# Performance work log

Measured on AMD Instinct MI355X. Metric: run time of the kernel, lower is better.

The kernel has to match this reference:

```python
import jax, jax.numpy as jnp
import numpy as np

D_MODEL, H, D_K, D_V, M = 1024, 8, 128, 128, 16
B, NQ, NK = 8, 1024, 1024


def setup_inputs() -> dict:
    key = jax.random.key(0)
    ks = jax.random.split(key, 12)
    f = jnp.float32
    inp = {
        "queries": jax.random.normal(ks[0], (B, NQ, D_MODEL), f),
        "keys": jax.random.normal(ks[1], (B, NK, D_MODEL), f),
        "values": jax.random.normal(ks[2], (B, NK, D_MODEL), f),
        "attention_mask": jax.random.bernoulli(ks[3], 0.15, (B, H, NQ, NK)),
        # linear weights stored (in, out) so y = x @ W + b
        "Wq": jax.random.normal(ks[4], (D_MODEL, H * D_K), f) * (2.0 / D_MODEL) ** 0.5,
        "bq": jnp.zeros((H * D_K,), f),
        "Wk": jax.random.normal(ks[5], (D_MODEL, H * D_K), f) * (2.0 / D_MODEL) ** 0.5,
        "bk": jnp.zeros((H * D_K,), f),
        "Wv": jax.random.normal(ks[6], (D_MODEL, H * D_V), f) * (2.0 / D_MODEL) ** 0.5,
        "bv": jnp.zeros((H * D_V,), f),
        "Wo": jax.random.normal(ks[7], (H * D_V, D_MODEL), f) * (2.0 / D_MODEL) ** 0.5,
        "bo": jnp.zeros((D_MODEL,), f),
        "m_k": jax.random.normal(ks[8], (1, M, H * D_K), f) * (1.0 / D_K),
        "m_v": jax.random.normal(ks[9], (1, M, H * D_V), f) * (1.0 / M),
    }
    return inp


def reference(queries, keys, values, attention_mask, Wq, bq, Wk, bk, Wv, bv, Wo, bo, m_k, m_v):
    b, nq, _ = queries.shape
    nk = keys.shape[1]
    scale = 1.0 / np.sqrt(D_K).astype(np.float32)

    q = (queries @ Wq + bq).reshape(b, nq, H, D_K)                # (b,nq,h,dk)
    mk = np.sqrt(D_K).astype(np.float32) * jnp.broadcast_to(m_k, (b, M, H * D_K))
    mv = np.sqrt(M).astype(np.float32) * jnp.broadcast_to(m_v, (b, M, H * D_V))
    k = jnp.concatenate([keys @ Wk + bk, mk], axis=1).reshape(b, nk + M, H, D_K)
    v = jnp.concatenate([values @ Wv + bv, mv], axis=1).reshape(b, nk + M, H, D_V)

    att = jnp.einsum("bqhd,bkhd->bhqk", q, k) * scale             # (b,h,nq,nk+m)
    # mask only the real-key slice; memory slots are never masked
    full_mask = jnp.concatenate(
        [attention_mask, jnp.zeros((b, H, nq, M), dtype=bool)], axis=-1)
    att = jnp.where(full_mask, -jnp.inf, att)
    att = jax.nn.softmax(att, axis=-1)

    out = jnp.einsum("bhqk,bkhd->bqhd", att, v).reshape(b, nq, H * D_V)
    out = out @ Wo + bo
    return out, att.reshape(-1, nq, nk)
```

## Files before the change

### kernel.cpp

```cpp
#include <hip/hip_runtime.h>


typedef unsigned short u16;
typedef unsigned int   u32;
typedef _Float16 f16x8 __attribute__((ext_vector_type(8)));
typedef short    s16x8 __attribute__((ext_vector_type(8)));
typedef float    f32x4 __attribute__((ext_vector_type(4)));

#define MFMA_F16(a, b, c) __builtin_amdgcn_mfma_f32_16x16x32_f16((a), (b), (c), 0, 0, 0)

#define NQS    1024
#define NKM    1040
#define KSP    1056
#define SCALE_QK 0.088388347648318447f

__device__ __forceinline__ u16 f2h(float f) {
  _Float16 h = (_Float16)f;
  return __builtin_bit_cast(u16, h);
}
__device__ __forceinline__ f16x8 ld_h8(const u16* p) {
  s16x8 r = *(const s16x8*)p;
  return __builtin_bit_cast(f16x8, r);
}

__global__ void cvt16_kernel(const float* __restrict__ in, u16* __restrict__ out, int n4) {
  for (int i = blockIdx.x * blockDim.x + threadIdx.x; i < n4;
       i += gridDim.x * blockDim.x) {
    float4 v = ((const float4*)in)[i];
    ushort4 h;
    h.x = f2h(v.x); h.y = f2h(v.y); h.z = f2h(v.z); h.w = f2h(v.w);
    ((ushort4*)out)[i] = h;
  }
}

__global__ __launch_bounds__(256)
void wtrans16_kernel(const float* __restrict__ w, u16* __restrict__ t16) {
  __shared__ float t[64][65];
  const int bx = blockIdx.x & 15;
  const int by = blockIdx.x >> 4;
  const int r = threadIdx.x >> 4, c4 = threadIdx.x & 15;
#pragma unroll
  for (int i = 0; i < 4; ++i) {
    const int row = bx * 64 + r + i * 16;
    float4 v = *(const float4*)&w[row * 1024 + by * 64 + c4 * 4];
    t[r + i * 16][c4 * 4 + 0] = v.x;
    t[r + i * 16][c4 * 4 + 1] = v.y;
    t[r + i * 16][c4 * 4 + 2] = v.z;
    t[r + i * 16][c4 * 4 + 3] = v.w;
  }
  __syncthreads();
  const int l = threadIdx.x & 63, og = threadIdx.x >> 6;
#pragma unroll
  for (int j = 0; j < 16; ++j) {
    const int o_local = og + j * 4;
    t16[(by * 64 + o_local) * 1024 + bx * 64 + l] = f2h(t[l][o_local]);
  }
}

__global__ void mk_fill_kernel(const float* __restrict__ m_k, u16* __restrict__ kh) {
  int idx = blockIdx.x * 256 + threadIdx.x;
  int b = idx >> 15, h = (idx >> 12) & 7, ko = (idx >> 7) & 31, dk = idx & 127;
  float v = 0.f;
  if (ko < 16) v = 11.313708498984760f * m_k[ko * 1024 + h * 128 + dk];
  kh[((b * 8 + h) * KSP + 1024 + ko) * 128 + dk] = f2h(v);
}

__global__ void mv_fill_kernel(const float* __restrict__ m_v, u16* __restrict__ vt) {
  int idx = blockIdx.x * 256 + threadIdx.x;
  int b = idx >> 15, h = (idx >> 12) & 7, dv = (idx >> 5) & 127, ko = idx & 31;
  float v = (ko < 16) ? 4.0f * m_v[ko * 1024 + h * 128 + dv] : 0.f;
  vt[((b * 8 + h) * 128 + dv) * KSP + 1024 + ko] = f2h(v);
}

__global__ void maskbits_kernel(const int* __restrict__ mask, u32* __restrict__ mbits) {
  const int lane = threadIdx.x & 63;
  const int nwave = (gridDim.x * blockDim.x) >> 6;
  int wid = (blockIdx.x * blockDim.x + threadIdx.x) >> 6;
  for (int g = wid; g < 262144; g += nwave) {
    const int4 m = *(const int4*)&mask[(size_t)g * 256 + lane * 4];
    u32 nib = (m.x ? 1u : 0u) | (m.y ? 2u : 0u) | (m.z ? 4u : 0u) | (m.w ? 8u : 0u);
    u32 v = nib << ((lane & 7) * 4);
    v |= __shfl_xor(v, 1);
    v |= __shfl_xor(v, 2);
    v |= __shfl_xor(v, 4);
    if ((lane & 7) == 0) {
      const int row = g >> 2;
      const int word = ((g & 3) << 3) + (lane >> 3);
      mbits[row * 33 + word] = v;
    }
  }
}

__global__ void maskfill_kernel(u32* __restrict__ mbits) {
  int idx = blockIdx.x * 256 + threadIdx.x;
  mbits[idx * 33 + 32] = 0xFFFF0000u;
}

__device__ __forceinline__ void stage_tile(const u16* __restrict__ gbase,
                                           u16* sbase, int w, int lane) {
#pragma unroll
  for (int i = 0; i < 4; ++i) {
    const u16* src = gbase + (w * 32 + i * 8 + (lane >> 3)) * 1024 + (lane & 7) * 8;
    u16* dst = sbase + (w * 32 + i * 8) * 64;
    __builtin_amdgcn_global_load_lds(
        (const __attribute__((address_space(1))) void*)src,
        (__attribute__((address_space(3))) void*)dst, 16, 0, 0);
  }
}

enum { EPI_Q16 = 0, EPI_K16 = 1, EPI_VT = 2, EPI_OUT = 3 };

template <int EPI>
__global__ __launch_bounds__(256)
void gemm_kernel(const u16* __restrict__ A, const u16* __restrict__ B,
                 const float* __restrict__ bias,
                 u16* __restrict__ oH, float* __restrict__ oF) {
  __shared__ u16 sA[128 * 64];
  __shared__ u16 sB[128 * 64];
  const int lane = threadIdx.x & 63, w = threadIdx.x >> 6;
  const int bm = blockIdx.x & 63, bn = blockIdx.x >> 6;
  const int wr = w >> 1, wc = w & 1;

  f32x4 acc[4][4];
  const f32x4 fz = {0.f, 0.f, 0.f, 0.f};
#pragma unroll
  for (int m = 0; m < 4; ++m)
#pragma unroll
    for (int n = 0; n < 4; ++n) acc[m][n] = fz;

  for (int kt = 0; kt < 16; ++kt) {
    const int kb = kt * 64;
    stage_tile(A + bm * 128 * 1024 + kb, sA, w, lane);
    stage_tile(B + bn * 128 * 1024 + kb, sB, w, lane);
    __syncthreads();
    const int ro = lane & 15;
#pragma unroll
    for (int kk = 0; kk < 2; ++kk) {
      const int co = kk * 32 + (lane >> 4) * 8;
      f16x8 a[4], b[4];
#pragma unroll
      for (int m = 0; m < 4; ++m) a[m] = ld_h8(&sA[(wr * 64 + m * 16 + ro) * 64 + co]);
#pragma unroll
      for (int n = 0; n < 4; ++n) b[n] = ld_h8(&sB[(wc * 64 + n * 16 + ro) * 64 + co]);
#pragma unroll
      for (int m = 0; m < 4; ++m)
#pragma unroll
        for (int n = 0; n < 4; ++n)
          acc[m][n] = MFMA_F16(a[m], b[n], acc[m][n]);
    }
    __syncthreads();
  }

#pragma unroll
  for (int m = 0; m < 4; ++m)
#pragma unroll
    for (int n = 0; n < 4; ++n) {
      const int row0 = bm * 128 + wr * 64 + m * 16 + ((lane >> 4) << 2);
      const int col = bn * 128 + wc * 64 + n * 16 + (lane & 15);
      const float bv = bias[col];
#pragma unroll
      for (int r = 0; r < 4; ++r) {
        const float y = acc[m][n][r] + bv;
        const int row = row0 + r;
        if constexpr (EPI == EPI_Q16) {
          oH[row * 1024 + col] = f2h(y);
        } else if constexpr (EPI == EPI_K16) {
          const int b = row >> 10, key = row & 1023;
          oH[((b * 8 + (col >> 7)) * KSP + key) * 128 + (col & 127)] = f2h(y);
        } else if constexpr (EPI == EPI_VT) {
          const int b = row >> 10, key = row & 1023;
          oH[((b * 8 + (col >> 7)) * 128 + (col & 127)) * KSP + key] = f2h(y);
        } else {
          oF[row * 1024 + col] = y;
        }
      }
    }
}

__global__ __launch_bounds__(256, 4)
void attn_kernel(const u16* __restrict__ qh, const u16* __restrict__ kh,
                 const u16* __restrict__ vt, const u32* __restrict__ mbits,
                 float* __restrict__ att, u16* __restrict__ obuf) {
  __shared__ __align__(16) u16 sK[64 * 128];
  __shared__ __align__(16) u16 sVt[128 * 40];
  __shared__ __align__(16) float sAtt[4][16][36];
  const int tid = threadIdx.x;
  const int lane = tid & 63, w = tid >> 6;

  const int d = blockIdx.x;
  const int j = d >> 3;
  const int bh = (d & 7) * 8 + (j >> 4);
  const int qblk = j & 15;
  const int h = bh & 7;
  const int b = bh >> 3;
  const int qrow0 = qblk * 64 + w * 16;
  const int grow0 = b * NQS + qrow0;
  const int ro = lane & 15, go = lane >> 4;

  f16x8 qf[4];
#pragma unroll
  for (int kk = 0; kk < 4; ++kk)
    qf[kk] = ld_h8(&qh[(grow0 + ro) * 1024 + h * 128 + kk * 32 + go * 8]);

  const u16* khb = kh + (size_t)bh * KSP * 128;
  const u16* vtb = vt + (size_t)bh * 128 * KSP;
  const u32* mbb = mbits + (size_t)bh * NQS * 33;
  float* attb = att + (size_t)(bh * NQS + qrow0) * NKM;

  const int r_k  = tid >> 4;
  const int cb_k = (tid & 15) * 16;
  const u16* kp0 = khb + r_k * 128 + (cb_k >> 1);
  const int dk0 = r_k * 256 + (cb_k ^ ((r_k & 7) << 4));

  const f32x4 fz = {0.f, 0.f, 0.f, 0.f};
  float lsum[4] = {0.f, 0.f, 0.f, 0.f};

  {
    s16x8 ra = *(const s16x8*)(kp0);
    s16x8 rb = *(const s16x8*)(kp0 + 16 * 128);
    s16x8 rc = *(const s16x8*)(kp0 + 32 * 128);
    s16x8 rd = *(const s16x8*)(kp0 + 48 * 128);
    for (int c = 0; c < 16; ++c) {
      __syncthreads();
      *(s16x8*)((char*)sK + dk0)         = ra;
      *(s16x8*)((char*)sK + dk0 + 4096)  = rb;
      *(s16x8*)((char*)sK + dk0 + 8192)  = rc;
      *(s16x8*)((char*)sK + dk0 + 12288) = rd;
      if (c < 15) {
        const u16* p = kp0 + (c + 1) * 64 * 128;
        ra = *(const s16x8*)(p);
        rb = *(const s16x8*)(p + 16 * 128);
        rc = *(const s16x8*)(p + 32 * 128);
        rd = *(const s16x8*)(p + 48 * 128);
      } else {
        ra = *(const s16x8*)(kp0 + 1024 * 128);
        rb = *(const s16x8*)(kp0 + 1040 * 128);
      }
      __syncthreads();
      u32 mw0[4], mw1[4];
#pragma unroll
      for (int r = 0; r < 4; ++r) {
        const int row = qrow0 + (go << 2) + r;
        mw0[r] = mbb[row * 33 + 2 * c];
        mw1[r] = mbb[row * 33 + 2 * c + 1];
      }
#pragma unroll
      for (int t = 0; t < 4; ++t) {
        f32x4 s = fz;
        const int rr = t * 16 + ro;
        const int sw = (rr & 7) << 4;
        __builtin_amdgcn_s_setprio(1);
#pragma unroll
        for (int kk = 0; kk < 4; ++kk) {
          const int off = rr * 256 + ((kk * 64 + go * 16) ^ sw);
          s = MFMA_F16(qf[kk], ld_h8((const u16*)((const char*)sK + off)), s);
        }
        __builtin_amdgcn_s_setprio(0);
        const int bit = (t & 1) * 16 + ro;
#pragma unroll
        for (int r = 0; r < 4; ++r) {
          const u32 mw = (t < 2) ? mw0[r] : mw1[r];
          const bool dead = (mw >> bit) & 1;
          const float e = dead ? 0.f : __expf(s[r] * SCALE_QK);
          lsum[r] += e;
        }
      }
    }
    __syncthreads();
    *(s16x8*)((char*)sK + dk0)        = ra;
    *(s16x8*)((char*)sK + dk0 + 4096) = rb;
    __syncthreads();
    u32 mwt[4];
#pragma unroll
    for (int r = 0; r < 4; ++r)
      mwt[r] = mbb[(qrow0 + (go << 2) + r) * 33 + 32];
#pragma unroll
    for (int t = 0; t < 2; ++t) {
      f32x4 s = fz;
      const int rr = t * 16 + ro;
      const int sw = (rr & 7) << 4;
#pragma unroll
      for (int kk = 0; kk < 4; ++kk) {
        const int off = rr * 256 + ((kk * 64 + go * 16) ^ sw);
        s = MFMA_F16(qf[kk], ld_h8((const u16*)((const char*)sK + off)), s);
      }
      const int bit = t * 16 + ro;
#pragma unroll
      for (int r = 0; r < 4; ++r) {
        const bool dead = (mwt[r] >> bit) & 1;
        lsum[r] += dead ? 0.f : __expf(s[r] * SCALE_QK);
      }
    }
  }

  float inv[4];
#pragma unroll
  for (int r = 0; r < 4; ++r) {
    lsum[r] += __shfl_xor(lsum[r], 1);
    lsum[r] += __shfl_xor(lsum[r], 2);
    lsum[r] += __shfl_xor(lsum[r], 4);
    lsum[r] += __shfl_xor(lsum[r], 8);
    inv[r] = 1.0f / lsum[r];
  }

  f32x4 oacc[8];
#pragma unroll
  for (int n = 0; n < 8; ++n) oacc[n] = fz;

  int vr[3], vcs[3];
  bool vok[3];
#pragma unroll
  for (int p = 0; p < 3; ++p) {
    const int t = p * 256 + tid;
    vok[p] = (t < 640);
    const int rr = vok[p] ? (t / 5) : 0;
    const int m5 = t - rr * 5;
    vr[p] = rr;
    vcs[p] = (m5 == 4 || !vok[p]) ? 0 : m5 * 8;
  }

  s16x8 rkh0, rkh1, rv0, rv1, rv2;
  rkh0 = *(const s16x8*)(kp0);
  rkh1 = *(const s16x8*)(kp0 + 16 * 128);
  rv0 = *(const s16x8*)(vtb + (size_t)vr[0] * KSP + vcs[0]);
  rv1 = *(const s16x8*)(vtb + (size_t)vr[1] * KSP + vcs[1]);
  if (vok[2]) rv2 = *(const s16x8*)(vtb + (size_t)vr[2] * KSP + vcs[2]);

  for (int c = 0; c < 33; ++c) {
    const int kb = c * 32;
    __syncthreads();
    *(s16x8*)((char*)sK + dk0)        = rkh0;
    *(s16x8*)((char*)sK + dk0 + 4096) = rkh1;
    *(s16x8*)((char*)sVt + tid * 16)         = rv0;
    *(s16x8*)((char*)sVt + (256 + tid) * 16) = rv1;
    if (vok[2]) *(s16x8*)((char*)sVt + (512 + tid) * 16) = rv2;
    if (c < 32) {
      const int nkb = (c + 1) * 32;
      rkh0 = *(const s16x8*)(kp0 + nkb * 128);
      rkh1 = *(const s16x8*)(kp0 + (nkb + 16) * 128);
      rv0 = *(const s16x8*)(vtb + (size_t)vr[0] * KSP + nkb + vcs[0]);
      rv1 = *(const s16x8*)(vtb + (size_t)vr[1] * KSP + nkb + vcs[1]);
      if (vok[2]) rv2 = *(const s16x8*)(vtb + (size_t)vr[2] * KSP + nkb + vcs[2]);
    }
    __syncthreads();

    u32 mw[4];
#pragma unroll
    for (int r = 0; r < 4; ++r) mw[r] = mbb[(qrow0 + (go << 2) + r) * 33 + c];

#pragma unroll
    for (int t = 0; t < 2; ++t) {
      f32x4 s = fz;
      const int rr = t * 16 + ro;
      const int sw = (rr & 7) << 4;
      __builtin_amdgcn_s_setprio(1);
#pragma unroll
      for (int kk = 0; kk < 4; ++kk) {
        const int off = rr * 256 + ((kk * 64 + go * 16) ^ sw);
        s = MFMA_F16(qf[kk], ld_h8((const u16*)((const char*)sK + off)), s);
      }
      __builtin_amdgcn_s_setprio(0);
      const int key_in = t * 16 + ro;
#pragma unroll
      for (int r = 0; r < 4; ++r) {
        const int lrow = (go << 2) + r;
        const bool dead = (mw[r] >> key_in) & 1;
        const float e = dead ? 0.f : __expf(s[r] * SCALE_QK);
        sAtt[w][lrow][t * 16 + ro] = e * inv[r];
      }
    }

    {
      const int arow = lane >> 2, cg = lane & 3;
      if (kb + cg * 8 < NKM) {
        f32x4 v0 = *(const f32x4*)&sAtt[w][arow][cg * 8];
        f32x4 v1 = *(const f32x4*)&sAtt[w][arow][cg * 8 + 4];
        float* dst = attb + (size_t)arow * NKM + kb + cg * 8;
        *(f32x4*)dst = v0;
        *(f32x4*)(dst + 4) = v1;
      }
    }

    {
      f32x4 p0 = *(const f32x4*)&sAtt[w][ro][go * 8];
      f32x4 p1 = *(const f32x4*)&sAtt[w][ro][go * 8 + 4];
      f16x8 pa;
      pa[0] = (_Float16)p0[0]; pa[1] = (_Float16)p0[1];
      pa[2] = (_Float16)p0[2]; pa[3] = (_Float16)p0[3];
      pa[4] = (_Float16)p1[0]; pa[5] = (_Float16)p1[1];
      pa[6] = (_Float16)p1[2]; pa[7] = (_Float16)p1[3];
      __builtin_amdgcn_s_setprio(1);
#pragma unroll
      for (int n = 0; n < 8; ++n) {
        f16x8 vb = ld_h8((const u16*)((const char*)sVt + (n * 16 + ro) * 80 + go * 16));
        oacc[n] = MFMA_F16(pa, vb, oacc[n]);
      }
      __builtin_amdgcn_s_setprio(0);
    }
  }

#pragma unroll
  for (int n = 0; n < 8; ++n)
#pragma unroll
    for (int r = 0; r < 4; ++r)
      obuf[(grow0 + (go << 2) + r) * 1024 + h * 128 + n * 16 + ro] = f2h(oacc[n][r]);
}

extern "C" void kernel_launch(void* const* d_in, const int* in_sizes, int n_in,
                              void* d_out, int out_size, void* d_ws, size_t ws_size,
                              hipStream_t stream) {
  const float* queries = (const float*)d_in[0];
  const float* keys    = (const float*)d_in[1];
  const float* values  = (const float*)d_in[2];
  const int*   mask    = (const int*)d_in[3];
  const float* Wq = (const float*)d_in[4];
  const float* bq = (const float*)d_in[5];
  const float* Wk = (const float*)d_in[6];
  const float* bk = (const float*)d_in[7];
  const float* Wv = (const float*)d_in[8];
  const float* bv = (const float*)d_in[9];
  const float* Wo = (const float*)d_in[10];
  const float* bo = (const float*)d_in[11];
  const float* m_k = (const float*)d_in[12];
  const float* m_v = (const float*)d_in[13];

  if (ws_size < 135528448) return;

  char* ws = (char*)d_ws;
  u16* xq  = (u16*)(ws + 0);
  u16* xk  = (u16*)(ws + 16777216);
  u16* xv  = (u16*)(ws + 33554432);
  u16* wq  = (u16*)(ws + 50331648);
  u16* wk  = (u16*)(ws + 52428800);
  u16* wv  = (u16*)(ws + 54525952);
  u16* wo  = (u16*)(ws + 56623104);
  u16* q16 = (u16*)(ws + 58720256);
  u16* k16 = (u16*)(ws + 75497472);
  u16* vt  = (u16*)(ws + 92798976);
  u16* obuf= (u16*)(ws + 110100480);
  u32* mbits=(u32*)(ws + 126877696);

  float* out = (float*)d_out;
  float* att = out + 8388608;

  cvt16_kernel<<<2048, 256, 0, stream>>>(queries, xq, 2097152);
  cvt16_kernel<<<2048, 256, 0, stream>>>(keys,    xk, 2097152);
  cvt16_kernel<<<2048, 256, 0, stream>>>(values,  xv, 2097152);
  wtrans16_kernel<<<256, 256, 0, stream>>>(Wq, wq);
  wtrans16_kernel<<<256, 256, 0, stream>>>(Wk, wk);
  wtrans16_kernel<<<256, 256, 0, stream>>>(Wv, wv);
  wtrans16_kernel<<<256, 256, 0, stream>>>(Wo, wo);
  gemm_kernel<EPI_Q16><<<512, 256, 0, stream>>>(xq, wq, bq, q16, nullptr);
  gemm_kernel<EPI_K16><<<512, 256, 0, stream>>>(xk, wk, bk, k16, nullptr);
  gemm_kernel<EPI_VT> <<<512, 256, 0, stream>>>(xv, wv, bv, vt,  nullptr);
  maskbits_kernel<<<2048, 256, 0, stream>>>(mask, mbits);
  maskfill_kernel<<<256, 256, 0, stream>>>(mbits);
  mk_fill_kernel<<<1024, 256, 0, stream>>>(m_k, k16);
  mv_fill_kernel<<<1024, 256, 0, stream>>>(m_v, vt);
  attn_kernel<<<1024, 256, 0, stream>>>(q16, k16, vt, mbits, att, obuf);
  gemm_kernel<EPI_OUT><<<512, 256, 0, stream>>>(obuf, wo, bo, nullptr, out);
}
```

Baseline: 409.5 us.

## Use 64-key chunks in attention PV pass and pad keys to uniform tiles

Pads the key dimension to 1088 and the mask row stride to 34 words, so both attention passes run 17 uniform 64-key chunks with no special tail block. The second pass now stages 64 keys of K and V per barrier pair instead of 32, halving the number of block synchronisations. The output tile is staged through LDS so the obuf stores become 16-byte writes. The extra registers and LDS lower the occupancy hint from 4 to 3 blocks per CU, and the padding adds some wasted MFMA work on masked-out keys.

```diff
diff --git a/kernel.cpp b/kernel.cpp
--- a/kernel.cpp
+++ b/kernel.cpp
@@ -11,7 +11,8 @@
 
 #define NQS    1024
 #define NKM    1040
-#define KSP    1056
+#define KSP    1088
+#define MW     34
 #define SCALE_QK 0.088388347648318447f
 
 __device__ __forceinline__ u16 f2h(float f) {
@@ -59,17 +60,19 @@
 
 __global__ void mk_fill_kernel(const float* __restrict__ m_k, u16* __restrict__ kh) {
   int idx = blockIdx.x * 256 + threadIdx.x;
-  int b = idx >> 15, h = (idx >> 12) & 7, ko = (idx >> 7) & 31, dk = idx & 127;
+  int bh = idx >> 13, ko = (idx >> 7) & 63, dk = idx & 127;
+  int h = bh & 7;
   float v = 0.f;
   if (ko < 16) v = 11.313708498984760f * m_k[ko * 1024 + h * 128 + dk];
-  kh[((b * 8 + h) * KSP + 1024 + ko) * 128 + dk] = f2h(v);
+  kh[((size_t)bh * KSP + 1024 + ko) * 128 + dk] = f2h(v);
 }
 
 __global__ void mv_fill_kernel(const float* __restrict__ m_v, u16* __restrict__ vt) {
   int idx = blockIdx.x * 256 + threadIdx.x;
-  int b = idx >> 15, h = (idx >> 12) & 7, dv = (idx >> 5) & 127, ko = idx & 31;
+  int bh = idx >> 13, dv = (idx >> 6) & 127, ko = idx & 63;
+  int h = bh & 7;
   float v = (ko < 16) ? 4.0f * m_v[ko * 1024 + h * 128 + dv] : 0.f;
-  vt[((b * 8 + h) * 128 + dv) * KSP + 1024 + ko] = f2h(v);
+  vt[((size_t)bh * 128 + dv) * KSP + 1024 + ko] = f2h(v);
 }
 
 __global__ void maskbits_kernel(const int* __restrict__ mask, u32* __restrict__ mbits) {
@@ -86,14 +89,15 @@
     if ((lane & 7) == 0) {
       const int row = g >> 2;
       const int word = ((g & 3) << 3) + (lane >> 3);
-      mbits[row * 33 + word] = v;
+      mbits[row * MW + word] = v;
     }
   }
 }
 
 __global__ void maskfill_kernel(u32* __restrict__ mbits) {
   int idx = blockIdx.x * 256 + threadIdx.x;
-  mbits[idx * 33 + 32] = 0xFFFF0000u;
+  mbits[idx * MW + 32] = 0xFFFF0000u;
+  mbits[idx * MW + 33] = 0xFFFFFFFFu;
 }
 
 __device__ __forceinline__ void stage_tile(const u16* __restrict__ gbase,
@@ -166,10 +170,10 @@
           oH[row * 1024 + col] = f2h(y);
         } else if constexpr (EPI == EPI_K16) {
           const int b = row >> 10, key = row & 1023;
-          oH[((b * 8 + (col >> 7)) * KSP + key) * 128 + (col & 127)] = f2h(y);
+          oH[((size_t)(b * 8 + (col >> 7)) * KSP + key) * 128 + (col & 127)] = f2h(y);
         } else if constexpr (EPI == EPI_VT) {
           const int b = row >> 10, key = row & 1023;
-          oH[((b * 8 + (col >> 7)) * 128 + (col & 127)) * KSP + key] = f2h(y);
+          oH[((size_t)(b * 8 + (col >> 7)) * 128 + (col & 127)) * KSP + key] = f2h(y);
         } else {
           oF[row * 1024 + col] = y;
         }
@@ -177,12 +181,12 @@
     }
 }
 
-__global__ __launch_bounds__(256, 4)
+__global__ __launch_bounds__(256, 3)
 void attn_kernel(const u16* __restrict__ qh, const u16* __restrict__ kh,
                  const u16* __restrict__ vt, const u32* __restrict__ mbits,
                  float* __restrict__ att, u16* __restrict__ obuf) {
   __shared__ __align__(16) u16 sK[64 * 128];
-  __shared__ __align__(16) u16 sVt[128 * 40];
+  __shared__ __align__(16) u16 sV[128 * 72];
   __shared__ __align__(16) float sAtt[4][16][36];
   const int tid = threadIdx.x;
   const int lane = tid & 63, w = tid >> 6;
@@ -204,45 +208,46 @@
 
   const u16* khb = kh + (size_t)bh * KSP * 128;
   const u16* vtb = vt + (size_t)bh * 128 * KSP;
-  const u32* mbb = mbits + (size_t)bh * NQS * 33;
+  const u32* mbb = mbits + (size_t)bh * NQS * MW;
   float* attb = att + (size_t)(bh * NQS + qrow0) * NKM;
 
   const int r_k  = tid >> 4;
   const int cb_k = (tid & 15) * 16;
   const u16* kp0 = khb + r_k * 128 + (cb_k >> 1);
   const int dk0 = r_k * 256 + (cb_k ^ ((r_k & 7) << 4));
+  const int vrow[4] = {(0 * 256 + tid) >> 3, (1 * 256 + tid) >> 3,
+                       (2 * 256 + tid) >> 3, (3 * 256 + tid) >> 3};
+  const int vc8[4]  = {(0 * 256 + tid) & 7, (1 * 256 + tid) & 7,
+                       (2 * 256 + tid) & 7, (3 * 256 + tid) & 7};
 
   const f32x4 fz = {0.f, 0.f, 0.f, 0.f};
   float lsum[4] = {0.f, 0.f, 0.f, 0.f};
 
   {
-    s16x8 ra = *(const s16x8*)(kp0);
-    s16x8 rb = *(const s16x8*)(kp0 + 16 * 128);
-    s16x8 rc = *(const s16x8*)(kp0 + 32 * 128);
-    s16x8 rd = *(const s16x8*)(kp0 + 48 * 128);
-    for (int c = 0; c < 16; ++c) {
+    s16x8 rk0 = *(const s16x8*)(kp0);
+    s16x8 rk1 = *(const s16x8*)(kp0 + 16 * 128);
+    s16x8 rk2 = *(const s16x8*)(kp0 + 32 * 128);
+    s16x8 rk3 = *(const s16x8*)(kp0 + 48 * 128);
+    for (int c = 0; c < 17; ++c) {
       __syncthreads();
-      *(s16x8*)((char*)sK + dk0)         = ra;
-      *(s16x8*)((char*)sK + dk0 + 4096)  = rb;
-      *(s16x8*)((char*)sK + dk0 + 8192)  = rc;
-      *(s16x8*)((char*)sK + dk0 + 12288) = rd;
-      if (c < 15) {
+      *(s16x8*)((char*)sK + dk0)         = rk0;
+      *(s16x8*)((char*)sK + dk0 + 4096)  = rk1;
+      *(s16x8*)((char*)sK + dk0 + 8192)  = rk2;
+      *(s16x8*)((char*)sK + dk0 + 12288) = rk3;
+      if (c < 16) {
         const u16* p = kp0 + (c + 1) * 64 * 128;
-        ra = *(const s16x8*)(p);
-        rb = *(const s16x8*)(p + 16 * 128);
-        rc = *(const s16x8*)(p + 32 * 128);
-        rd = *(const s16x8*)(p + 48 * 128);
-      } else {
-        ra = *(const s16x8*)(kp0 + 1024 * 128);
-        rb = *(const s16x8*)(kp0 + 1040 * 128);
+        rk0 = *(const s16x8*)(p);
+        rk1 = *(const s16x8*)(p + 16 * 128);
+        rk2 = *(const s16x8*)(p + 32 * 128);
+        rk3 = *(const s16x8*)(p + 48 * 128);
       }
       __syncthreads();
       u32 mw0[4], mw1[4];
 #pragma unroll
       for (int r = 0; r < 4; ++r) {
         const int row = qrow0 + (go << 2) + r;
-        mw0[r] = mbb[row * 33 + 2 * c];
-        mw1[r] = mbb[row * 33 + 2 * c + 1];
+        mw0[r] = mbb[row * MW + 2 * c];
+        mw1[r] = mbb[row * MW + 2 * c + 1];
       }
 #pragma unroll
       for (int t = 0; t < 4; ++t) {
@@ -261,34 +266,8 @@
         for (int r = 0; r < 4; ++r) {
           const u32 mw = (t < 2) ? mw0[r] : mw1[r];
           const bool dead = (mw >> bit) & 1;
-          const float e = dead ? 0.f : __expf(s[r] * SCALE_QK);
-          lsum[r] += e;
-        }
-      }
-    }
-    __syncthreads();
-    *(s16x8*)((char*)sK + dk0)        = ra;
-    *(s16x8*)((char*)sK + dk0 + 4096) = rb;
-    __syncthreads();
-    u32 mwt[4];
-#pragma unroll
-    for (int r = 0; r < 4; ++r)
-      mwt[r] = mbb[(qrow0 + (go << 2) + r) * 33 + 32];
-#pragma unroll
-    for (int t = 0; t < 2; ++t) {
-      f32x4 s = fz;
-      const int rr = t * 16 + ro;
-      const int sw = (rr & 7) << 4;
-#pragma unroll
-      for (int kk = 0; kk < 4; ++kk) {
-        const int off = rr * 256 + ((kk * 64 + go * 16) ^ sw);
-        s = MFMA_F16(qf[kk], ld_h8((const u16*)((const char*)sK + off)), s);
-      }
-      const int bit = t * 16 + ro;
-#pragma unroll
-      for (int r = 0; r < 4; ++r) {
-        const bool dead = (mwt[r] >> bit) & 1;
-        lsum[r] += dead ? 0.f : __expf(s[r] * SCALE_QK);
+          lsum[r] += dead ? 0.f : __expf(s[r] * SCALE_QK);
+        }
       }
     }
   }
@@ -307,103 +286,118 @@
 #pragma unroll
   for (int n = 0; n < 8; ++n) oacc[n] = fz;
 
-  int vr[3], vcs[3];
-  bool vok[3];
-#pragma unroll
-  for (int p = 0; p < 3; ++p) {
-    const int t = p * 256 + tid;
-    vok[p] = (t < 640);
-    const int rr = vok[p] ? (t / 5) : 0;
-    const int m5 = t - rr * 5;
-    vr[p] = rr;
-    vcs[p] = (m5 == 4 || !vok[p]) ? 0 : m5 * 8;
-  }
-
-  s16x8 rkh0, rkh1, rv0, rv1, rv2;
-  rkh0 = *(const s16x8*)(kp0);
-  rkh1 = *(const s16x8*)(kp0 + 16 * 128);
-  rv0 = *(const s16x8*)(vtb + (size_t)vr[0] * KSP + vcs[0]);
-  rv1 = *(const s16x8*)(vtb + (size_t)vr[1] * KSP + vcs[1]);
-  if (vok[2]) rv2 = *(const s16x8*)(vtb + (size_t)vr[2] * KSP + vcs[2]);
-
-  for (int c = 0; c < 33; ++c) {
-    const int kb = c * 32;
+  s16x8 rk0 = *(const s16x8*)(kp0);
+  s16x8 rk1 = *(const s16x8*)(kp0 + 16 * 128);
+  s16x8 rk2 = *(const s16x8*)(kp0 + 32 * 128);
+  s16x8 rk3 = *(const s16x8*)(kp0 + 48 * 128);
+  s16x8 rv0 = *(const s16x8*)(vtb + (size_t)vrow[0] * KSP + vc8[0] * 8);
+  s16x8 rv1 = *(const s16x8*)(vtb + (size_t)vrow[1] * KSP + vc8[1] * 8);
+  s16x8 rv2 = *(const s16x8*)(vtb + (size_t)vrow[2] * KSP + vc8[2] * 8);
+  s16x8 rv3 = *(const s16x8*)(vtb + (size_t)vrow[3] * KSP + vc8[3] * 8);
+
+  for (int c = 0; c < 17; ++c) {
     __syncthreads();
-    *(s16x8*)((char*)sK + dk0)        = rkh0;
-    *(s16x8*)((char*)sK + dk0 + 4096) = rkh1;
-    *(s16x8*)((char*)sVt + tid * 16)         = rv0;
-    *(s16x8*)((char*)sVt + (256 + tid) * 16) = rv1;
-    if (vok[2]) *(s16x8*)((char*)sVt + (512 + tid) * 16) = rv2;
-    if (c < 32) {
-      const int nkb = (c + 1) * 32;
-      rkh0 = *(const s16x8*)(kp0 + nkb * 128);
-      rkh1 = *(const s16x8*)(kp0 + (nkb + 16) * 128);
-      rv0 = *(const s16x8*)(vtb + (size_t)vr[0] * KSP + nkb + vcs[0]);
-      rv1 = *(const s16x8*)(vtb + (size_t)vr[1] * KSP + nkb + vcs[1]);
-      if (vok[2]) rv2 = *(const s16x8*)(vtb + (size_t)vr[2] * KSP + nkb + vcs[2]);
+    *(s16x8*)((char*)sK + dk0)         = rk0;
+    *(s16x8*)((char*)sK + dk0 + 4096)  = rk1;
+    *(s16x8*)((char*)sK + dk0 + 8192)  = rk2;
+    *(s16x8*)((char*)sK + dk0 + 12288) = rk3;
+    *(s16x8*)((char*)sV + vrow[0] * 144 + vc8[0] * 16) = rv0;
+    *(s16x8*)((char*)sV + vrow[1] * 144 + vc8[1] * 16) = rv1;
+    *(s16x8*)((char*)sV + vrow[2] * 144 + vc8[2] * 16) = rv2;
+    *(s16x8*)((char*)sV + vrow[3] * 144 + vc8[3] * 16) = rv3;
+    if (c < 16) {
+      const int nkb = (c + 1) * 64;
+      const u16* p = kp0 + nkb * 128;
+      rk0 = *(const s16x8*)(p);
+      rk1 = *(const s16x8*)(p + 16 * 128);
+      rk2 = *(const s16x8*)(p + 32 * 128);
+      rk3 = *(const s16x8*)(p + 48 * 128);
+      rv0 = *(const s16x8*)(vtb + (size_t)vrow[0] * KSP + nkb + vc8[0] * 8);
+      rv1 = *(const s16x8*)(vtb + (size_t)vrow[1] * KSP + nkb + vc8[1] * 8);
+      rv2 = *(const s16x8*)(vtb + (size_t)vrow[2] * KSP + nkb + vc8[2] * 8);
+      rv3 = *(const s16x8*)(vtb + (size_t)vrow[3] * KSP + nkb + vc8[3] * 8);
     }
     __syncthreads();
 
-    u32 mw[4];
-#pragma unroll
-    for (int r = 0; r < 4; ++r) mw[r] = mbb[(qrow0 + (go << 2) + r) * 33 + c];
-
-#pragma unroll
-    for (int t = 0; t < 2; ++t) {
-      f32x4 s = fz;
-      const int rr = t * 16 + ro;
-      const int sw = (rr & 7) << 4;
-      __builtin_amdgcn_s_setprio(1);
-#pragma unroll
-      for (int kk = 0; kk < 4; ++kk) {
-        const int off = rr * 256 + ((kk * 64 + go * 16) ^ sw);
-        s = MFMA_F16(qf[kk], ld_h8((const u16*)((const char*)sK + off)), s);
-      }
-      __builtin_amdgcn_s_setprio(0);
-      const int key_in = t * 16 + ro;
-#pragma unroll
-      for (int r = 0; r < 4; ++r) {
-        const int lrow = (go << 2) + r;
-        const bool dead = (mw[r] >> key_in) & 1;
-        const float e = dead ? 0.f : __expf(s[r] * SCALE_QK);
-        sAtt[w][lrow][t * 16 + ro] = e * inv[r];
-      }
-    }
-
-    {
-      const int arow = lane >> 2, cg = lane & 3;
-      if (kb + cg * 8 < NKM) {
-        f32x4 v0 = *(const f32x4*)&sAtt[w][arow][cg * 8];
-        f32x4 v1 = *(const f32x4*)&sAtt[w][arow][cg * 8 + 4];
-        float* dst = attb + (size_t)arow * NKM + kb + cg * 8;
-        *(f32x4*)dst = v0;
-        *(f32x4*)(dst + 4) = v1;
-      }
-    }
-
-    {
-      f32x4 p0 = *(const f32x4*)&sAtt[w][ro][go * 8];
-      f32x4 p1 = *(const f32x4*)&sAtt[w][ro][go * 8 + 4];
-      f16x8 pa;
-      pa[0] = (_Float16)p0[0]; pa[1] = (_Float16)p0[1];
-      pa[2] = (_Float16)p0[2]; pa[3] = (_Float16)p0[3];
-      pa[4] = (_Float16)p1[0]; pa[5] = (_Float16)p1[1];
-      pa[6] = (_Float16)p1[2]; pa[7] = (_Float16)p1[3];
-      __builtin_amdgcn_s_setprio(1);
-#pragma unroll
-      for (int n = 0; n < 8; ++n) {
-        f16x8 vb = ld_h8((const u16*)((const char*)sVt + (n * 16 + ro) * 80 + go * 16));
-        oacc[n] = MFMA_F16(pa, vb, oacc[n]);
-      }
-      __builtin_amdgcn_s_setprio(0);
-    }
-  }
-
-#pragma unroll
-  for (int n = 0; n < 8; ++n)
-#pragma unroll
-    for (int r = 0; r < 4; ++r)
-      obuf[(grow0 + (go << 2) + r) * 1024 + h * 128 + n * 16 + ro] = f2h(oacc[n][r]);
+    u32 mwc[2][4];
+#pragma unroll
+    for (int r = 0; r < 4; ++r) {
+      const int row = qrow0 + (go << 2) + r;
+      mwc[0][r] = mbb[row * MW + 2 * c];
+      mwc[1][r] = mbb[row * MW + 2 * c + 1];
+    }
+
+#pragma unroll
+    for (int t2 = 0; t2 < 2; ++t2) {
+#pragma unroll
+      for (int t = 0; t < 2; ++t) {
+        f32x4 s = fz;
+        const int rr = t2 * 32 + t * 16 + ro;
+        const int sw = (rr & 7) << 4;
+        __builtin_amdgcn_s_setprio(1);
+#pragma unroll
+        for (int kk = 0; kk < 4; ++kk) {
+          const int off = rr * 256 + ((kk * 64 + go * 16) ^ sw);
+          s = MFMA_F16(qf[kk], ld_h8((const u16*)((const char*)sK + off)), s);
+        }
+        __builtin_amdgcn_s_setprio(0);
+        const int bit = t * 16 + ro;
+#pragma unroll
+        for (int r = 0; r < 4; ++r) {
+          const int lrow = (go << 2) + r;
+          const bool dead = (mwc[t2][r] >> bit) & 1;
+          const float e = dead ? 0.f : __expf(s[r] * SCALE_QK);
+          sAtt[w][lrow][t * 16 + ro] = e * inv[r];
+        }
+      }
+
+      {
+        const int kbh = c * 64 + t2 * 32;
+        const int arow = lane >> 2, cg = lane & 3;
+        if (kbh + cg * 8 < NKM) {
+          f32x4 v0 = *(const f32x4*)&sAtt[w][arow][cg * 8];
+          f32x4 v1 = *(const f32x4*)&sAtt[w][arow][cg * 8 + 4];
+          float* dst = attb + (size_t)arow * NKM + kbh + cg * 8;
+          *(f32x4*)dst = v0;
+          *(f32x4*)(dst + 4) = v1;
+        }
+      }
+
+      {
+        f32x4 p0 = *(const f32x4*)&sAtt[w][ro][go * 8];
+        f32x4 p1 = *(const f32x4*)&sAtt[w][ro][go * 8 + 4];
+        f16x8 pa;
+        pa[0] = (_Float16)p0[0]; pa[1] = (_Float16)p0[1];
+        pa[2] = (_Float16)p0[2]; pa[3] = (_Float16)p0[3];
+        pa[4] = (_Float16)p1[0]; pa[5] = (_Float16)p1[1];
+        pa[6] = (_Float16)p1[2]; pa[7] = (_Float16)p1[3];
+        __builtin_amdgcn_s_setprio(1);
+#pragma unroll
+        for (int n = 0; n < 8; ++n) {
+          f16x8 vb = ld_h8((const u16*)((const char*)sV + (n * 16 + ro) * 144 + t2 * 64 + go * 16));
+          oacc[n] = MFMA_F16(pa, vb, oacc[n]);
+        }
+        __builtin_amdgcn_s_setprio(0);
+      }
+    }
+  }
+
+  __syncthreads();
+  {
+    u16* os = (u16*)((char*)sK + w * 4096);
+#pragma unroll
+    for (int n = 0; n < 8; ++n)
+#pragma unroll
+      for (int r = 0; r < 4; ++r)
+        os[((go << 2) + r) * 128 + n * 16 + ro] = f2h(oacc[n][r]);
+#pragma unroll
+    for (int i = 0; i < 4; ++i) {
+      const int idx = i * 64 + lane;
+      const int row = idx >> 4, c16 = idx & 15;
+      s16x8 v = *(const s16x8*)(os + row * 128 + c16 * 8);
+      *(s16x8*)&obuf[(size_t)(grow0 + row) * 1024 + h * 128 + c16 * 8] = v;
+    }
+  }
 }
 
 extern "C" void kernel_launch(void* const* d_in, const int* in_sizes, int n_in,
@@ -424,7 +418,7 @@
   const float* m_k = (const float*)d_in[12];
   const float* m_v = (const float*)d_in[13];
 
-  if (ws_size < 135528448) return;
+  if (ws_size < 136839168) return;
 
   char* ws = (char*)d_ws;
   u16* xq  = (u16*)(ws + 0);
@@ -436,9 +430,9 @@
   u16* wo  = (u16*)(ws + 56623104);
   u16* q16 = (u16*)(ws + 58720256);
   u16* k16 = (u16*)(ws + 75497472);
-  u16* vt  = (u16*)(ws + 92798976);
-  u16* obuf= (u16*)(ws + 110100480);
-  u32* mbits=(u32*)(ws + 126877696);
+  u16* vt  = (u16*)(ws + 93323264);
+  u16* obuf= (u16*)(ws + 111149056);
+  u32* mbits=(u32*)(ws + 127926272);
 
   float* out = (float*)d_out;
   float* att = out + 8388608;
@@ -455,8 +449,8 @@
   gemm_kernel<EPI_VT> <<<512, 256, 0, stream>>>(xv, wv, bv, vt,  nullptr);
   maskbits_kernel<<<2048, 256, 0, stream>>>(mask, mbits);
   maskfill_kernel<<<256, 256, 0, stream>>>(mbits);
-  mk_fill_kernel<<<1024, 256, 0, stream>>>(m_k, k16);
-  mv_fill_kernel<<<1024, 256, 0, stream>>>(m_v, vt);
+  mk_fill_kernel<<<2048, 256, 0, stream>>>(m_k, k16);
+  mv_fill_kernel<<<2048, 256, 0, stream>>>(m_v, vt);
   attn_kernel<<<1024, 256, 0, stream>>>(q16, k16, vt, mbits, att, obuf);
   gemm_kernel<EPI_OUT><<<512, 256, 0, stream>>>(obuf, wo, bo, nullptr, out);
 }
```

Measured after the change: 406.2 us. No clear change (-0.8%).
